# Kernel optimization log

Measured on AMD Instinct MI355X. Metric: run time of the kernel, lower is better.

Reference implementation:

```python
import jax, jax.numpy as jnp
import numpy as np

ALPHA = 0.2
N_ENT, N_TYP, N_REL, E = 100000, 1000, 200, 500000
D = 64          # nfeat1 = nfeat2 = nhid1 = nhid2 = relation_dim
NHEADS = 2      # forced by the tuple-unpack in the original forward


def _xavier(key, shape):
    fan_out, fan_in = shape[0], shape[-1]
    lim = 1.414 * np.sqrt(6.0 / (fan_in + fan_out))
    return jax.random.uniform(key, shape, jnp.float32, -lim, lim)


def setup_inputs() -> dict:
    key = jax.random.key(0)
    ks = jax.random.split(key, 32)
    inp = {
        "entity_embeddings": jax.random.normal(ks[0], (N_ENT, D), jnp.float32),
        "type_embed": jax.random.normal(ks[1], (N_TYP, D), jnp.float32),
        "relation_embed": jax.random.normal(ks[2], (N_REL, D), jnp.float32),
        "edge_list": jax.random.randint(ks[3], (2, E), 0, N_TYP),  # row0=src entity, row1=dst type; both in-range
        "edge_type": jax.random.randint(ks[4], (E,), 0, N_REL),
        "edge_embed": jax.random.normal(ks[5], (E, D), jnp.float32),
    }
    Din = 3 * D  # cat(x1[src], x2[dst], edge_embed)
    i = 6
    for h in range(NHEADS):
        inp[f"a_e{h}"] = _xavier(ks[i], (D, Din)); i += 1   # entity-side attention proj
        inp[f"v_e{h}"] = _xavier(ks[i], (1, D))[0]; i += 1  # entity-side score vector
        inp[f"a_t{h}"] = _xavier(ks[i], (D, Din)); i += 1   # type-side attention proj
        inp[f"v_t{h}"] = _xavier(ks[i], (1, D))[0]; i += 1
    Ho = NHEADS * D       # 128
    Dout = 3 * Ho         # out layer input cat dim
    inp["a_eo"] = _xavier(ks[i], (Ho, Dout)); i += 1
    inp["v_eo"] = _xavier(ks[i], (1, Ho))[0]; i += 1
    inp["a_to"] = _xavier(ks[i], (Ho, Dout)); i += 1
    inp["v_to"] = _xavier(ks[i], (1, Ho))[0]; i += 1
    inp["W"] = _xavier(ks[i], (D, Ho))  # relation_dim -> nheads*nhid1
    return inp


def _gat_e2t(x1, x2, src, dst, e, a_e, v_e, a_t, v_t, concat):
    """Bipartite sparse GAT layer (KBGAT-style, e2t variant).
    Message m = a @ cat(x1[src], x2[dst], edge_embed); score = exp(-leaky_relu(v . m));
    softmax-normalized scatter-aggregate to entity nodes (by src) and type nodes (by dst)."""
    d1, d2 = x1.shape[1], x2.shape[1]

    def agg(a, v, seg, nseg):
        a1, a2, a3 = a[:, :d1], a[:, d1:d1 + d2], a[:, d1 + d2:]
        # project nodes first, then gather (avoids materializing [E, 3d] cat)
        m = (x1 @ a1.T)[src] + (x2 @ a2.T)[dst] + e @ a3.T     # [E, h]
        s = jnp.exp(-jax.nn.leaky_relu(m @ v, ALPHA))          # [E] unnormalized attention
        num = jax.ops.segment_sum(m * s[:, None], seg, num_segments=nseg)
        den = jax.ops.segment_sum(s, seg, num_segments=nseg)
        h = num / jnp.where(den == 0, 1.0, den)[:, None]
        return jax.nn.elu(h) if concat else h

    h_e = agg(a_e, v_e, src, x1.shape[0])
    h_t = agg(a_t, v_t, dst, x2.shape[0])
    return h_e, h_t


def reference(entity_embeddings, type_embed, relation_embed, edge_list, edge_type, edge_embed,
              a_e0, v_e0, a_t0, v_t0, a_e1, v_e1, a_t1, v_t1,
              a_eo, v_eo, a_to, v_to, W):
    src, dst = edge_list[0], edge_list[1]
    # two attention heads (concat=True -> elu inside)
    h0e, h0t = _gat_e2t(entity_embeddings, type_embed, src, dst, edge_embed, a_e0, v_e0, a_t0, v_t0, True)
    h1e, h1t = _gat_e2t(entity_embeddings, type_embed, src, dst, edge_embed, a_e1, v_e1, a_t1, v_t1, True)
    x1 = jnp.concatenate([h0e, h1e], axis=1)  # [N_ENT, 2*nhid1]
    x2 = jnp.concatenate([h0t, h1t], axis=1)  # [N_TYP, 2*nhid2]
    # dropout is identity at inference
    out_rel = relation_embed @ W              # [N_REL, nheads*nhid1]
    e2 = out_rel[edge_type]                   # per-edge relation embedding
    o1, o2 = _gat_e2t(x1, x2, src, dst, e2, a_eo, v_eo, a_to, v_to, False)
    return jax.nn.elu(o1), jax.nn.elu(o2), out_rel
```

## Files before the change

### kernel.cpp

```cpp
#include <hip/hip_runtime.h>

#define ALPHA 0.2f
#define NT 1000
#define NRELC 200
#define NE 500000
#define N_ENT 100000
#define CH 4096
#define G 123

static constexpr size_t I_STARTS_SRC = 0;
static constexpr size_t I_STARTS_DST = 1001;
static constexpr size_t I_COLSUM     = 2002;
static constexpr size_t I_HIST2      = 4002;
static constexpr size_t I_BASE2      = 250002;
static constexpr size_t I_AB_SRC     = 496002;
static constexpr size_t I_AB_DST     = 1496002;

static constexpr size_t F_U1 = 2496004;
static constexpr size_t F_U2 = F_U1 + 768;
static constexpr size_t F_L1 = F_U2 + 768;
static constexpr size_t F_X1 = F_L1 + 4*130000;
static constexpr size_t F_X2 = F_X1 + 128000;
static constexpr size_t F_OR = F_X2 + 128000;
static constexpr size_t F_L2 = F_OR + 25600;
static constexpr size_t S2F = 283800;
static constexpr size_t WS_FLOATS = F_L2 + 2*S2F;

static constexpr size_t OUT_O2  = 12800000;
static constexpr size_t OUT_REL = 12928000;

__device__ __forceinline__ float eluf(float x) { return x > 0.f ? x : expm1f(x); }
__device__ __forceinline__ float scoref(float slin) {
  return expf(slin > 0.f ? -slin : -ALPHA * slin);
}

__global__ __launch_bounds__(256) void k_hist2(const int* __restrict__ src,
                                               const int* __restrict__ dst,
                                               int* __restrict__ ip) {
  __shared__ int h[NT];
  int bid = blockIdx.x;
  int side = bid >= G;
  int blk = bid - side * G;
  const int* keys = side ? dst : src;
  int j0 = blk * CH;
  int n = min(CH, NE - j0);
  for (int i = threadIdx.x; i < NT; i += 256) h[i] = 0;
  __syncthreads();
  for (int k = threadIdx.x; k < n; k += 256) atomicAdd(&h[keys[j0 + k]], 1);
  __syncthreads();
  int* row = ip + I_HIST2 + (size_t)(side * G + blk) * NT;
  for (int b = threadIdx.x; b < NT; b += 256) row[b] = h[b];
}

__global__ void k_colsum(int* __restrict__ ip) {
  int t = blockIdx.x * 256 + threadIdx.x;
  if (t >= 2 * NT) return;
  int side = t / NT, bin = t - side * NT;
  int s = 0;
  for (int blk = 0; blk < G; ++blk)
    s += ip[I_HIST2 + (size_t)(side * G + blk) * NT + bin];
  ip[I_COLSUM + t] = s;
}

__global__ void k_scan2b(int* __restrict__ ip) {
  __shared__ int buf[1024];
  int t = threadIdx.x;
  for (int side = 0; side < 2; ++side) {
    int v = (t < NT) ? ip[I_COLSUM + side * NT + t] : 0;
    buf[t] = v;
    __syncthreads();
    for (int off = 1; off < 1024; off <<= 1) {
      int x = (t >= off) ? buf[t - off] : 0;
      __syncthreads();
      buf[t] += x;
      __syncthreads();
    }
    int* st = ip + (side ? I_STARTS_DST : I_STARTS_SRC);
    if (t < NT) st[t] = buf[t] - v;
    if (t == NT - 1) st[NT] = buf[t];
    __syncthreads();
  }
}

__global__ void k_bases(int* __restrict__ ip) {
  int t = blockIdx.x * 256 + threadIdx.x;
  if (t >= 2 * NT) return;
  int side = t / NT, bin = t - side * NT;
  int run = ip[(side ? I_STARTS_DST : I_STARTS_SRC) + bin];
  for (int blk = 0; blk < G; ++blk) {
    size_t idx = I_HIST2 + (size_t)(side * G + blk) * NT + bin;
    int c = ip[idx];
    ip[idx + (I_BASE2 - I_HIST2)] = run;
    run += c;
  }
}

__global__ __launch_bounds__(256) void k_binscat(const int* __restrict__ src,
                                                 const int* __restrict__ dst,
                                                 const int* __restrict__ et,
                                                 int* __restrict__ ip) {
  __shared__ int2 bufs[CH];
  __shared__ int loff[1024];
  __shared__ int lcur[1024];
  __shared__ int gbase[1024];
  __shared__ int psum[256];
  int bid = blockIdx.x;
  int side = bid >= G;
  int blk = bid - side * G;
  const int* keys = side ? dst : src;
  const int* oths = side ? src : dst;
  int j0 = blk * CH;
  int n = min(CH, NE - j0);
  int t = threadIdx.x;

  for (int i = t; i < 1024; i += 256) lcur[i] = 0;
  __syncthreads();
  for (int k = t; k < n; k += 256) atomicAdd(&lcur[keys[j0 + k]], 1);
  __syncthreads();
  int c0 = lcur[4*t], c1 = lcur[4*t+1], c2 = lcur[4*t+2], c3 = lcur[4*t+3];
  int s = c0 + c1 + c2 + c3;
  psum[t] = s;
  __syncthreads();
  for (int off = 1; off < 256; off <<= 1) {
    int x = (t >= off) ? psum[t - off] : 0;
    __syncthreads();
    psum[t] += x;
    __syncthreads();
  }
  int base = psum[t] - s;
  loff[4*t]   = base;
  loff[4*t+1] = base + c0;
  loff[4*t+2] = base + c0 + c1;
  loff[4*t+3] = base + c0 + c1 + c2;
  lcur[4*t]   = loff[4*t];
  lcur[4*t+1] = loff[4*t+1];
  lcur[4*t+2] = loff[4*t+2];
  lcur[4*t+3] = loff[4*t+3];
  const int* brow = ip + I_BASE2 + (size_t)(side * G + blk) * NT;
  for (int b = t; b < NT; b += 256) gbase[b] = brow[b];
  __syncthreads();
  for (int k = t; k < n; k += 256) {
    int j = j0 + k;
    int b = keys[j];
    int pos = atomicAdd(&lcur[b], 1);
    bufs[pos] = make_int2(j | (b << 19), oths[j] | (et[j] << 16));
  }
  __syncthreads();
  int2* out = reinterpret_cast<int2*>(ip + (side ? I_AB_DST : I_AB_SRC));
  for (int k = t; k < n; k += 256) {
    int2 q = bufs[k];
    int b = q.x >> 19;
    int posg = gbase[b] + (k - loff[b]);
    out[posg] = make_int2(q.x & 0x7FFFF, q.y);
  }
}

__global__ void k_prep_u(const float* aE0, const float* vE0, const float* aT0, const float* vT0,
                         const float* aE1, const float* vE1, const float* aT1, const float* vT1,
                         const float* aEo, const float* vEo, const float* aTo, const float* vTo,
                         float* ws) {
  int t = blockIdx.x * blockDim.x + threadIdx.x;
  if (t < 768) {
    int c = t / 192, rem = t - c*192;
    int p = rem >> 6, k = rem & 63;
    const float* a = (c==0)?aE0:(c==1)?aT0:(c==2)?aE1:aT1;
    const float* v = (c==0)?vE0:(c==1)?vT0:(c==2)?vE1:vT1;
    float s = 0.f;
    for (int o = 0; o < 64; ++o) s += a[o*192 + p*64 + k] * v[o];
    ws[F_U1 + (size_t)(c*3+p)*64 + k] = s;
  } else if (t < 1536) {
    int tt = t - 768;
    int c = tt / 384, rem = tt - c*384;
    int p = rem >> 7, k = rem & 127;
    const float* a = c ? aTo : aEo;
    const float* v = c ? vTo : vEo;
    float s = 0.f;
    for (int o = 0; o < 128; ++o) s += a[o*384 + p*128 + k] * v[o];
    ws[F_U2 + (size_t)(c*3+p)*128 + k] = s;
  }
}

__global__ __launch_bounds__(256) void k_l1_proj(const float* Ent, const float* Typ,
                                                 const float* aE0, const float* aT0,
                                                 const float* aE1, const float* aT1,
                                                 float* ws) {
  int bid = blockIdx.x;
  int t = threadIdx.x;
  if (bid < 504) {
    __shared__ float xs[16][64];
    int c = bid / 126, rem = bid - c*126;
    int table = rem / 63, tile = rem - table*63;
    int i0 = tile * 16;
    const float* a = (c==0)?aE0:(c==1)?aT0:(c==2)?aE1:aT1;
    const float* x = table ? Typ : Ent;
    float* outb = ws + F_L1 + (size_t)c*130000 + (table ? 64000 : 0);
    for (int idx = t; idx < 1024; idx += 256) {
      int r = idx >> 6, k = idx & 63;
      int i = i0 + r;
      xs[r][k] = (i < NT) ? x[(size_t)i*64 + k] : 0.f;
    }
    __syncthreads();
    int o = t & 63, grp = t >> 6;
    const float* arow = a + o*192 + table*64;
    float acc0 = 0.f, acc1 = 0.f, acc2 = 0.f, acc3 = 0.f;
    #pragma unroll 8
    for (int k = 0; k < 64; ++k) {
      float av = arow[k];
      acc0 += xs[grp*4+0][k] * av;
      acc1 += xs[grp*4+1][k] * av;
      acc2 += xs[grp*4+2][k] * av;
      acc3 += xs[grp*4+3][k] * av;
    }
    int ib = i0 + grp*4;
    if (ib + 0 < NT) outb[(size_t)(ib+0)*64 + o] = acc0;
    if (ib + 1 < NT) outb[(size_t)(ib+1)*64 + o] = acc1;
    if (ib + 2 < NT) outb[(size_t)(ib+2)*64 + o] = acc2;
    if (ib + 3 < NT) outb[(size_t)(ib+3)*64 + o] = acc3;
  } else {
    int idx = (bid - 504) * 256 + t;
    if (idx >= 8000) return;
    int c = idx / 2000, rem = idx - c*2000;
    float* base = ws + F_L1 + (size_t)c * 130000;
    if (rem < 1000) {
      const float* x = Ent + (size_t)rem*64;
      const float* u = ws + F_U1 + (size_t)(c*3)*64;
      float s = 0.f;
      #pragma unroll
      for (int k = 0; k < 64; ++k) s += x[k]*u[k];
      base[128000 + rem] = s;
    } else {
      int i = rem - 1000;
      const float* x = Typ + (size_t)i*64;
      const float* u = ws + F_U1 + (size_t)(c*3+1)*64;
      float s = 0.f;
      #pragma unroll
      for (int k = 0; k < 64; ++k) s += x[k]*u[k];
      base[129000 + i] = s;
    }
  }
}

__global__ __launch_bounds__(256) void k_l1_acc(const float* __restrict__ Eemb,
                                                const float* aE0, const float* aT0,
                                                const float* aE1, const float* aT1,
                                                const int* __restrict__ ip,
                                                float* __restrict__ ws) {
  __shared__ float Tl[2][NT];
  __shared__ float cOthL[2][NT];
  __shared__ float accR[2][16][64];
  __shared__ float accE[2][64];
  __shared__ float red[256];
  __shared__ float denl[2];

  int side = blockIdx.x >= NT;
  int g = blockIdx.x - side * NT;
  int t = threadIdx.x;
  int sub = t & 15, slot = t >> 4;
  int c0 = side, c1 = side + 2;

  size_t othOff = side ? 128000 : 129000;
  size_t ownOff = side ? 129000 : 128000;
  for (int i = t; i < NT; i += 256) {
    Tl[0][i] = 0.f; Tl[1][i] = 0.f;
    cOthL[0][i] = ws[F_L1 + (size_t)c0*130000 + othOff + i];
    cOthL[1][i] = ws[F_L1 + (size_t)c1*130000 + othOff + i];
  }
  if (t < 2) denl[t] = 0.f;
  float ownA = ws[F_L1 + (size_t)c0*130000 + ownOff + g];
  float ownB = ws[F_L1 + (size_t)c1*130000 + ownOff + g];
  float4 w3A = reinterpret_cast<const float4*>(ws + F_U1 + (size_t)(c0*3+2)*64)[sub];
  float4 w3B = reinterpret_cast<const float4*>(ws + F_U1 + (size_t)(c1*3+2)*64)[sub];
  __syncthreads();

  int start = ip[(side ? I_STARTS_DST : I_STARTS_SRC) + g];
  int end   = ip[(side ? I_STARTS_DST : I_STARTS_SRC) + g + 1];
  const int2* ab = reinterpret_cast<const int2*>(ip + (side ? I_AB_DST : I_AB_SRC));
  const float4* EV = reinterpret_cast<const float4*>(Eemb);

  float4 acc0 = make_float4(0.f,0.f,0.f,0.f);
  float4 acc1 = make_float4(0.f,0.f,0.f,0.f);
  float d0 = 0.f, d1 = 0.f;

  int p = start + slot;
  for (; p + 48 < end; p += 64) {
    int2 q0 = ab[p], q1 = ab[p+16], q2 = ab[p+32], q3 = ab[p+48];
    float4 e0 = EV[(size_t)q0.x*16 + sub];
    float4 e1 = EV[(size_t)q1.x*16 + sub];
    float4 e2 = EV[(size_t)q2.x*16 + sub];
    float4 e3 = EV[(size_t)q3.x*16 + sub];
    float rA0 = e0.x*w3A.x + e0.y*w3A.y + e0.z*w3A.z + e0.w*w3A.w;
    float rB0 = e0.x*w3B.x + e0.y*w3B.y + e0.z*w3B.z + e0.w*w3B.w;
    float rA1 = e1.x*w3A.x + e1.y*w3A.y + e1.z*w3A.z + e1.w*w3A.w;
    float rB1 = e1.x*w3B.x + e1.y*w3B.y + e1.z*w3B.z + e1.w*w3B.w;
    float rA2 = e2.x*w3A.x + e2.y*w3A.y + e2.z*w3A.z + e2.w*w3A.w;
    float rB2 = e2.x*w3B.x + e2.y*w3B.y + e2.z*w3B.z + e2.w*w3B.w;
    float rA3 = e3.x*w3A.x + e3.y*w3A.y + e3.z*w3A.z + e3.w*w3A.w;
    float rB3 = e3.x*w3B.x + e3.y*w3B.y + e3.z*w3B.z + e3.w*w3B.w;
    #pragma unroll
    for (int sh = 1; sh < 16; sh <<= 1) {
      rA0 += __shfl_xor(rA0, sh, 16); rB0 += __shfl_xor(rB0, sh, 16);
      rA1 += __shfl_xor(rA1, sh, 16); rB1 += __shfl_xor(rB1, sh, 16);
      rA2 += __shfl_xor(rA2, sh, 16); rB2 += __shfl_xor(rB2, sh, 16);
      rA3 += __shfl_xor(rA3, sh, 16); rB3 += __shfl_xor(rB3, sh, 16);
    }
    int o0 = q0.y & 0xFFFF, o1 = q1.y & 0xFFFF, o2 = q2.y & 0xFFFF, o3 = q3.y & 0xFFFF;
    float sA0 = scoref(ownA + cOthL[0][o0] + rA0);
    float sB0 = scoref(ownB + cOthL[1][o0] + rB0);
    float sA1 = scoref(ownA + cOthL[0][o1] + rA1);
    float sB1 = scoref(ownB + cOthL[1][o1] + rB1);
    float sA2 = scoref(ownA + cOthL[0][o2] + rA2);
    float sB2 = scoref(ownB + cOthL[1][o2] + rB2);
    float sA3 = scoref(ownA + cOthL[0][o3] + rA3);
    float sB3 = scoref(ownB + cOthL[1][o3] + rB3);
    acc0.x += sA0*e0.x + sA1*e1.x + sA2*e2.x + sA3*e3.x;
    acc0.y += sA0*e0.y + sA1*e1.y + sA2*e2.y + sA3*e3.y;
    acc0.z += sA0*e0.z + sA1*e1.z + sA2*e2.z + sA3*e3.z;
    acc0.w += sA0*e0.w + sA1*e1.w + sA2*e2.w + sA3*e3.w;
    acc1.x += sB0*e0.x + sB1*e1.x + sB2*e2.x + sB3*e3.x;
    acc1.y += sB0*e0.y + sB1*e1.y + sB2*e2.y + sB3*e3.y;
    acc1.z += sB0*e0.z + sB1*e1.z + sB2*e2.z + sB3*e3.z;
    acc1.w += sB0*e0.w + sB1*e1.w + sB2*e2.w + sB3*e3.w;
    if (sub == 0) {
      atomicAdd(&Tl[0][o0], sA0); atomicAdd(&Tl[1][o0], sB0);
      atomicAdd(&Tl[0][o1], sA1); atomicAdd(&Tl[1][o1], sB1);
      atomicAdd(&Tl[0][o2], sA2); atomicAdd(&Tl[1][o2], sB2);
      atomicAdd(&Tl[0][o3], sA3); atomicAdd(&Tl[1][o3], sB3);
      d0 += sA0 + sA1 + sA2 + sA3;
      d1 += sB0 + sB1 + sB2 + sB3;
    }
  }
  for (; p < end; p += 16) {
    int2 q = ab[p];
    float4 ev = EV[(size_t)q.x*16 + sub];
    float rA = ev.x*w3A.x + ev.y*w3A.y + ev.z*w3A.z + ev.w*w3A.w;
    float rB = ev.x*w3B.x + ev.y*w3B.y + ev.z*w3B.z + ev.w*w3B.w;
    #pragma unroll
    for (int sh = 1; sh < 16; sh <<= 1) {
      rA += __shfl_xor(rA, sh, 16);
      rB += __shfl_xor(rB, sh, 16);
    }
    int oth = q.y & 0xFFFF;
    float sA = scoref(ownA + cOthL[0][oth] + rA);
    float sB = scoref(ownB + cOthL[1][oth] + rB);
    acc0.x += sA*ev.x; acc0.y += sA*ev.y; acc0.z += sA*ev.z; acc0.w += sA*ev.w;
    acc1.x += sB*ev.x; acc1.y += sB*ev.y; acc1.z += sB*ev.z; acc1.w += sB*ev.w;
    if (sub == 0) {
      atomicAdd(&Tl[0][oth], sA);
      atomicAdd(&Tl[1][oth], sB);
      d0 += sA; d1 += sB;
    }
  }
  *reinterpret_cast<float4*>(&accR[0][slot][sub*4]) = acc0;
  *reinterpret_cast<float4*>(&accR[1][slot][sub*4]) = acc1;
  if (sub == 0) { atomicAdd(&denl[0], d0); atomicAdd(&denl[1], d1); }
  __syncthreads();
  if (t < 128) {
    int ci = t >> 6, o = t & 63;
    float s = 0.f;
    #pragma unroll
    for (int sl = 0; sl < 16; ++sl) s += accR[ci][sl][o];
    accE[ci][o] = s;
  }
  __syncthreads();

  int o = t & 63, part = t >> 6;
  size_t othPOff = side ? 0 : 64000;
  size_t ownPOff = side ? 64000 : 0;
  #pragma unroll
  for (int ci = 0; ci < 2; ++ci) {
    int c = side + 2*ci;
    const float* Pc = ws + F_L1 + (size_t)c * 130000;
    const float* Poth = Pc + othPOff;
    float sum = 0.f;
    for (int dd = part*250; dd < part*250 + 250; ++dd)
      sum += Tl[ci][dd] * Poth[(size_t)dd*64 + o];
    red[t] = sum;
    __syncthreads();
    if (part == 0) {
      sum = red[o] + red[64+o] + red[128+o] + red[192+o];
      const float* a = (c==0)?aE0:(c==1)?aT0:(c==2)?aE1:aT1;
      const float* a3 = a + o*192 + 128;
      float acc = 0.f;
      #pragma unroll
      for (int k = 0; k < 64; ++k) acc += accE[ci][k]*a3[k];
      float den = denl[ci];
      float own = Pc[ownPOff + (size_t)g*64 + o];
      float num = sum + acc + den*own;
      float h = num / (den == 0.f ? 1.f : den);
      float* dst = ws + (side ? F_X2 : F_X1);
      dst[(size_t)g*128 + ci*64 + o] = eluf(h);
    }
    __syncthreads();
  }
}

__global__ void k_relW(const float* Rel, const float* W, float* ws, float* dout) {
  int t = blockIdx.x * blockDim.x + threadIdx.x;
  if (t >= NRELC*128) return;
  int r = t >> 7, o = t & 127;
  const float* x = Rel + (size_t)r*64;
  float s = 0.f;
  #pragma unroll
  for (int k = 0; k < 64; ++k) s += x[k] * W[(size_t)k*128 + o];
  ws[F_OR + t] = s;
  dout[OUT_REL + t] = s;
}

__global__ __launch_bounds__(256) void k_l2_proj(const float* aEo, const float* aTo,
                                                 float* ws) {
  int bid = blockIdx.x;
  int t = threadIdx.x;
  const float* x1 = ws + F_X1;
  const float* x2 = ws + F_X2;
  const float* orel = ws + F_OR;
  if (bid < 278) {
    __shared__ float xs[16][128];
    int c = bid / 139, rem = bid - c*139;
    const float* a = c ? aTo : aEo;
    float* cb = ws + F_L2 + (size_t)c * S2F;
    const float* x; int part, tile, nrows; float* outb;
    if (rem < 63)       { x = x1;   part = 0; tile = rem;       nrows = NT;    outb = cb; }
    else if (rem < 126) { x = x2;   part = 1; tile = rem - 63;  nrows = NT;    outb = cb + 128000; }
    else                { x = orel; part = 2; tile = rem - 126; nrows = NRELC; outb = cb + 256000; }
    int i0 = tile * 16;
    for (int idx = t; idx < 2048; idx += 256) {
      int r = idx >> 7, k = idx & 127;
      int i = i0 + r;
      xs[r][k] = (i < nrows) ? x[(size_t)i*128 + k] : 0.f;
    }
    __syncthreads();
    int o = t & 127, grp = t >> 7;
    const float* arow = a + (size_t)o*384 + part*128;
    float acc[8] = {0.f,0.f,0.f,0.f,0.f,0.f,0.f,0.f};
    #pragma unroll 4
    for (int k = 0; k < 128; ++k) {
      float av = arow[k];
      #pragma unroll
      for (int r = 0; r < 8; ++r)
        acc[r] += xs[grp*8+r][k] * av;
    }
    int ib = i0 + grp*8;
    #pragma unroll
    for (int r = 0; r < 8; ++r)
      if (ib + r < nrows) outb[(size_t)(ib+r)*128 + o] = acc[r];
  } else {
    int idx = (bid - 278) * 256 + t;
    if (idx >= 4400) return;
    int c = idx / 2200, rem = idx - c*2200;
    float* base = ws + F_L2 + (size_t)c * S2F;
    if (rem < 1000) {
      const float* u = ws + F_U2 + (size_t)(c*3)*128;
      const float* x = x1 + (size_t)rem*128;
      float s = 0.f;
      for (int k = 0; k < 128; ++k) s += x[k]*u[k];
      base[281600 + rem] = s;
    } else if (rem < 2000) {
      int i = rem - 1000;
      const float* u = ws + F_U2 + (size_t)(c*3+1)*128;
      const float* x = x2 + (size_t)i*128;
      float s = 0.f;
      for (int k = 0; k < 128; ++k) s += x[k]*u[k];
      base[282600 + i] = s;
    } else {
      int r = rem - 2000;
      const float* u = ws + F_U2 + (size_t)(c*3+2)*128;
      const float* x = orel + (size_t)r*128;
      float s = 0.f;
      for (int k = 0; k < 128; ++k) s += x[k]*u[k];
      base[283600 + r] = s;
    }
  }
}

__global__ __launch_bounds__(256) void k_l2_seg(const int* __restrict__ ip,
                                                float* __restrict__ ws,
                                                float* __restrict__ dout) {
  __shared__ float Tl[NT];
  __shared__ float Ul[NRELC];
  __shared__ float cOthL[NT];
  __shared__ float cRelL[NRELC];
  __shared__ float red[256];
  __shared__ float denl;

  int c = blockIdx.x >= NT;
  int g = blockIdx.x - c * NT;
  int t = threadIdx.x;
  float* base = ws + F_L2 + (size_t)c * S2F;

  size_t othOff = c ? 281600 : 282600;
  size_t ownOff = c ? 282600 : 281600;
  for (int i = t; i < NT; i += 256) { Tl[i] = 0.f; cOthL[i] = base[othOff + i]; }
  for (int i = t; i < NRELC; i += 256) { Ul[i] = 0.f; cRelL[i] = base[283600 + i]; }
  if (t == 0) denl = 0.f;
  float own = base[ownOff + g];
  __syncthreads();

  int start = ip[(c ? I_STARTS_DST : I_STARTS_SRC) + g];
  int end   = ip[(c ? I_STARTS_DST : I_STARTS_SRC) + g + 1];
  const int2* ab = reinterpret_cast<const int2*>(ip + (c ? I_AB_DST : I_AB_SRC));

  float dpart = 0.f;
  for (int p = start + t; p < end; p += 256) {
    int2 q = ab[p];
    int oth = q.y & 0xFFFF;
    int r = q.y >> 16;
    float sv = scoref(own + cOthL[oth] + cRelL[r]);
    atomicAdd(&Tl[oth], sv);
    atomicAdd(&Ul[r], sv);
    dpart += sv;
  }
  atomicAdd(&denl, dpart);
  __syncthreads();

  int o = t & 127, part = t >> 7;
  const float* Qoth = base + (c ? 0 : 128000);
  const float* R3 = base + 256000;
  float sum = 0.f;
  for (int dd = part*500; dd < part*500 + 500; ++dd)
    sum += Tl[dd] * Qoth[(size_t)dd*128 + o];
  for (int rr = part*100; rr < part*100 + 100; ++rr)
    sum += Ul[rr] * R3[(size_t)rr*128 + o];
  red[t] = sum;
  __syncthreads();
  if (part == 0) {
    sum = red[o] + red[128+o];
    float den = denl;
    float ownQ = base[(c ? 128000 : 0) + (size_t)g*128 + o];
    float num = sum + den*ownQ;
    float h = num / (den == 0.f ? 1.f : den);
    size_t off = c ? (OUT_O2 + (size_t)g*128 + o) : ((size_t)g*128 + o);
    dout[off] = eluf(h);
  }
}

extern "C" void kernel_launch(void* const* d_in, const int* in_sizes, int n_in,
                              void* d_out, int out_size, void* d_ws, size_t ws_size,
                              hipStream_t stream) {
  (void)in_sizes; (void)n_in;
  const float* Ent = (const float*)d_in[0];
  const float* Typ = (const float*)d_in[1];
  const float* Rel = (const float*)d_in[2];
  const int*   edge = (const int*)d_in[3];
  const int*   etyp = (const int*)d_in[4];
  const float* Eemb = (const float*)d_in[5];
  const float* aE0 = (const float*)d_in[6];
  const float* vE0 = (const float*)d_in[7];
  const float* aT0 = (const float*)d_in[8];
  const float* vT0 = (const float*)d_in[9];
  const float* aE1 = (const float*)d_in[10];
  const float* vE1 = (const float*)d_in[11];
  const float* aT1 = (const float*)d_in[12];
  const float* vT1 = (const float*)d_in[13];
  const float* aEo = (const float*)d_in[14];
  const float* vEo = (const float*)d_in[15];
  const float* aTo = (const float*)d_in[16];
  const float* vTo = (const float*)d_in[17];
  const float* W   = (const float*)d_in[18];
  float* ws  = (float*)d_ws;
  int*   ip  = (int*)d_ws;
  float* out = (float*)d_out;
  const int* srcA = edge;
  const int* dstA = edge + NE;

  if (ws_size < WS_FLOATS * sizeof(float)) return;

  hipMemsetAsync(d_out, 0, (size_t)out_size * sizeof(float), stream);

  k_hist2  <<<2*G, 256, 0, stream>>>(srcA, dstA, ip);
  k_colsum <<<8, 256, 0, stream>>>(ip);
  k_scan2b <<<1, 1024, 0, stream>>>(ip);
  k_bases  <<<8, 256, 0, stream>>>(ip);
  k_binscat<<<2*G, 256, 0, stream>>>(srcA, dstA, etyp, ip);
  k_prep_u <<<6, 256, 0, stream>>>(aE0,vE0,aT0,vT0,aE1,vE1,aT1,vT1,aEo,vEo,aTo,vTo,ws);
  k_l1_proj<<<536, 256, 0, stream>>>(Ent, Typ, aE0, aT0, aE1, aT1, ws);
  k_l1_acc <<<2000, 256, 0, stream>>>(Eemb, aE0, aT0, aE1, aT1, ip, ws);
  k_relW   <<<100, 256, 0, stream>>>(Rel, W, ws, out);
  k_l2_proj<<<296, 256, 0, stream>>>(aEo, aTo, ws);
  k_l2_seg <<<2000, 256, 0, stream>>>(ip, ws, out);
}
```

Before: 262.5 us.

## Pair segments per block in layer-2 aggregation, alias shared memory, halve binning chunk

The layer-2 segment kernel now handles two adjacent nodes per block, so each projection row read from Qoth and R3 serves both nodes and the block count is halved. The layer-1 accumulation kernel reuses one flat shared buffer, with the reduction scratch overlapping the score tables after an extra barrier, which cuts LDS use and may allow more resident blocks. The binning chunk size is halved and the grid doubled, with workspace offsets moved to fit the larger histogram. The costs are an extra per-edge branch in layer 2, less parallelism when segments are small, and one more sync in layer 1.

```diff
diff --git a/kernel.cpp b/kernel.cpp
--- a/kernel.cpp
+++ b/kernel.cpp
@@ -5,18 +5,18 @@
 #define NRELC 200
 #define NE 500000
 #define N_ENT 100000
-#define CH 4096
-#define G 123
+#define CH 2048
+#define G 245
 
 static constexpr size_t I_STARTS_SRC = 0;
 static constexpr size_t I_STARTS_DST = 1001;
 static constexpr size_t I_COLSUM     = 2002;
 static constexpr size_t I_HIST2      = 4002;
-static constexpr size_t I_BASE2      = 250002;
-static constexpr size_t I_AB_SRC     = 496002;
-static constexpr size_t I_AB_DST     = 1496002;
-
-static constexpr size_t F_U1 = 2496004;
+static constexpr size_t I_BASE2      = 494002;
+static constexpr size_t I_AB_SRC     = 984002;
+static constexpr size_t I_AB_DST     = 1984002;
+
+static constexpr size_t F_U1 = 2984004;
 static constexpr size_t F_U2 = F_U1 + 768;
 static constexpr size_t F_L1 = F_U2 + 768;
 static constexpr size_t F_X1 = F_L1 + 4*130000;
@@ -245,12 +245,14 @@
                                                 const float* aE1, const float* aT1,
                                                 const int* __restrict__ ip,
                                                 float* __restrict__ ws) {
-  __shared__ float Tl[2][NT];
-  __shared__ float cOthL[2][NT];
-  __shared__ float accR[2][16][64];
-  __shared__ float accE[2][64];
-  __shared__ float red[256];
-  __shared__ float denl[2];
+  __shared__ float smem[4434];
+  float* TlB   = smem;
+  float* cOth0 = smem + 2000;
+  float* cOth1 = smem + 3000;
+  float* accRf = smem + 2000;
+  float* accEf = smem + 4048;
+  float* redf  = smem + 4176;
+  float* denf  = smem + 4432;
 
   int side = blockIdx.x >= NT;
   int g = blockIdx.x - side * NT;
@@ -261,11 +263,11 @@
   size_t othOff = side ? 128000 : 129000;
   size_t ownOff = side ? 129000 : 128000;
   for (int i = t; i < NT; i += 256) {
-    Tl[0][i] = 0.f; Tl[1][i] = 0.f;
-    cOthL[0][i] = ws[F_L1 + (size_t)c0*130000 + othOff + i];
-    cOthL[1][i] = ws[F_L1 + (size_t)c1*130000 + othOff + i];
-  }
-  if (t < 2) denl[t] = 0.f;
+    TlB[i] = 0.f; TlB[1000 + i] = 0.f;
+    cOth0[i] = ws[F_L1 + (size_t)c0*130000 + othOff + i];
+    cOth1[i] = ws[F_L1 + (size_t)c1*130000 + othOff + i];
+  }
+  if (t < 2) denf[t] = 0.f;
   float ownA = ws[F_L1 + (size_t)c0*130000 + ownOff + g];
   float ownB = ws[F_L1 + (size_t)c1*130000 + ownOff + g];
   float4 w3A = reinterpret_cast<const float4*>(ws + F_U1 + (size_t)(c0*3+2)*64)[sub];
@@ -304,14 +306,14 @@
       rA3 += __shfl_xor(rA3, sh, 16); rB3 += __shfl_xor(rB3, sh, 16);
     }
     int o0 = q0.y & 0xFFFF, o1 = q1.y & 0xFFFF, o2 = q2.y & 0xFFFF, o3 = q3.y & 0xFFFF;
-    float sA0 = scoref(ownA + cOthL[0][o0] + rA0);
-    float sB0 = scoref(ownB + cOthL[1][o0] + rB0);
-    float sA1 = scoref(ownA + cOthL[0][o1] + rA1);
-    float sB1 = scoref(ownB + cOthL[1][o1] + rB1);
-    float sA2 = scoref(ownA + cOthL[0][o2] + rA2);
-    float sB2 = scoref(ownB + cOthL[1][o2] + rB2);
-    float sA3 = scoref(ownA + cOthL[0][o3] + rA3);
-    float sB3 = scoref(ownB + cOthL[1][o3] + rB3);
+    float sA0 = scoref(ownA + cOth0[o0] + rA0);
+    float sB0 = scoref(ownB + cOth1[o0] + rB0);
+    float sA1 = scoref(ownA + cOth0[o1] + rA1);
+    float sB1 = scoref(ownB + cOth1[o1] + rB1);
+    float sA2 = scoref(ownA + cOth0[o2] + rA2);
+    float sB2 = scoref(ownB + cOth1[o2] + rB2);
+    float sA3 = scoref(ownA + cOth0[o3] + rA3);
+    float sB3 = scoref(ownB + cOth1[o3] + rB3);
     acc0.x += sA0*e0.x + sA1*e1.x + sA2*e2.x + sA3*e3.x;
     acc0.y += sA0*e0.y + sA1*e1.y + sA2*e2.y + sA3*e3.y;
     acc0.z += sA0*e0.z + sA1*e1.z + sA2*e2.z + sA3*e3.z;
@@ -321,10 +323,10 @@
     acc1.z += sB0*e0.z + sB1*e1.z + sB2*e2.z + sB3*e3.z;
     acc1.w += sB0*e0.w + sB1*e1.w + sB2*e2.w + sB3*e3.w;
     if (sub == 0) {
-      atomicAdd(&Tl[0][o0], sA0); atomicAdd(&Tl[1][o0], sB0);
-      atomicAdd(&Tl[0][o1], sA1); atomicAdd(&Tl[1][o1], sB1);
-      atomicAdd(&Tl[0][o2], sA2); atomicAdd(&Tl[1][o2], sB2);
-      atomicAdd(&Tl[0][o3], sA3); atomicAdd(&Tl[1][o3], sB3);
+      atomicAdd(&TlB[o0], sA0); atomicAdd(&TlB[1000+o0], sB0);
+      atomicAdd(&TlB[o1], sA1); atomicAdd(&TlB[1000+o1], sB1);
+      atomicAdd(&TlB[o2], sA2); atomicAdd(&TlB[1000+o2], sB2);
+      atomicAdd(&TlB[o3], sA3); atomicAdd(&TlB[1000+o3], sB3);
       d0 += sA0 + sA1 + sA2 + sA3;
       d1 += sB0 + sB1 + sB2 + sB3;
     }
@@ -340,26 +342,27 @@
       rB += __shfl_xor(rB, sh, 16);
     }
     int oth = q.y & 0xFFFF;
-    float sA = scoref(ownA + cOthL[0][oth] + rA);
-    float sB = scoref(ownB + cOthL[1][oth] + rB);
+    float sA = scoref(ownA + cOth0[oth] + rA);
+    float sB = scoref(ownB + cOth1[oth] + rB);
     acc0.x += sA*ev.x; acc0.y += sA*ev.y; acc0.z += sA*ev.z; acc0.w += sA*ev.w;
     acc1.x += sB*ev.x; acc1.y += sB*ev.y; acc1.z += sB*ev.z; acc1.w += sB*ev.w;
     if (sub == 0) {
-      atomicAdd(&Tl[0][oth], sA);
-      atomicAdd(&Tl[1][oth], sB);
+      atomicAdd(&TlB[oth], sA);
+      atomicAdd(&TlB[1000+oth], sB);
       d0 += sA; d1 += sB;
     }
   }
-  *reinterpret_cast<float4*>(&accR[0][slot][sub*4]) = acc0;
-  *reinterpret_cast<float4*>(&accR[1][slot][sub*4]) = acc1;
-  if (sub == 0) { atomicAdd(&denl[0], d0); atomicAdd(&denl[1], d1); }
+  __syncthreads();
+  *reinterpret_cast<float4*>(&accRf[slot*64 + sub*4])        = acc0;
+  *reinterpret_cast<float4*>(&accRf[1024 + slot*64 + sub*4]) = acc1;
+  if (sub == 0) { atomicAdd(&denf[0], d0); atomicAdd(&denf[1], d1); }
   __syncthreads();
   if (t < 128) {
     int ci = t >> 6, o = t & 63;
     float s = 0.f;
     #pragma unroll
-    for (int sl = 0; sl < 16; ++sl) s += accR[ci][sl][o];
-    accE[ci][o] = s;
+    for (int sl = 0; sl < 16; ++sl) s += accRf[ci*1024 + sl*64 + o];
+    accEf[ci*64 + o] = s;
   }
   __syncthreads();
 
@@ -373,17 +376,17 @@
     const float* Poth = Pc + othPOff;
     float sum = 0.f;
     for (int dd = part*250; dd < part*250 + 250; ++dd)
-      sum += Tl[ci][dd] * Poth[(size_t)dd*64 + o];
-    red[t] = sum;
+      sum += TlB[ci*1000 + dd] * Poth[(size_t)dd*64 + o];
+    redf[t] = sum;
     __syncthreads();
     if (part == 0) {
-      sum = red[o] + red[64+o] + red[128+o] + red[192+o];
+      sum = redf[o] + redf[64+o] + redf[128+o] + redf[192+o];
       const float* a = (c==0)?aE0:(c==1)?aT0:(c==2)?aE1:aT1;
       const float* a3 = a + o*192 + 128;
       float acc = 0.f;
       #pragma unroll
-      for (int k = 0; k < 64; ++k) acc += accE[ci][k]*a3[k];
-      float den = denl[ci];
+      for (int k = 0; k < 64; ++k) acc += accEf[ci*64 + k]*a3[k];
+      float den = denf[ci];
       float own = Pc[ownPOff + (size_t)g*64 + o];
       float num = sum + acc + den*own;
       float h = num / (den == 0.f ? 1.f : den);
@@ -475,62 +478,73 @@
 __global__ __launch_bounds__(256) void k_l2_seg(const int* __restrict__ ip,
                                                 float* __restrict__ ws,
                                                 float* __restrict__ dout) {
-  __shared__ float Tl[NT];
-  __shared__ float Ul[NRELC];
+  __shared__ float Tl[2][NT];
+  __shared__ float Ul[2][NRELC];
   __shared__ float cOthL[NT];
   __shared__ float cRelL[NRELC];
-  __shared__ float red[256];
-  __shared__ float denl;
-
-  int c = blockIdx.x >= NT;
-  int g = blockIdx.x - c * NT;
+  __shared__ float red[2][256];
+  __shared__ float denl[2];
+
+  int c = blockIdx.x >= 500;
+  int gp = blockIdx.x - c * 500;
+  int g0 = gp * 2;
   int t = threadIdx.x;
   float* base = ws + F_L2 + (size_t)c * S2F;
 
   size_t othOff = c ? 281600 : 282600;
   size_t ownOff = c ? 282600 : 281600;
-  for (int i = t; i < NT; i += 256) { Tl[i] = 0.f; cOthL[i] = base[othOff + i]; }
-  for (int i = t; i < NRELC; i += 256) { Ul[i] = 0.f; cRelL[i] = base[283600 + i]; }
-  if (t == 0) denl = 0.f;
-  float own = base[ownOff + g];
-  __syncthreads();
-
-  int start = ip[(c ? I_STARTS_DST : I_STARTS_SRC) + g];
-  int end   = ip[(c ? I_STARTS_DST : I_STARTS_SRC) + g + 1];
+  for (int i = t; i < NT; i += 256) { Tl[0][i] = 0.f; Tl[1][i] = 0.f; cOthL[i] = base[othOff + i]; }
+  for (int i = t; i < NRELC; i += 256) { Ul[0][i] = 0.f; Ul[1][i] = 0.f; cRelL[i] = base[283600 + i]; }
+  if (t < 2) denl[t] = 0.f;
+  float own0 = base[ownOff + g0];
+  float own1 = base[ownOff + g0 + 1];
+  __syncthreads();
+
+  const int* st = ip + (c ? I_STARTS_DST : I_STARTS_SRC);
+  int s0 = st[g0], split = st[g0 + 1], e1 = st[g0 + 2];
   const int2* ab = reinterpret_cast<const int2*>(ip + (c ? I_AB_DST : I_AB_SRC));
 
-  float dpart = 0.f;
-  for (int p = start + t; p < end; p += 256) {
+  float d0 = 0.f, d1 = 0.f;
+  for (int p = s0 + t; p < e1; p += 256) {
     int2 q = ab[p];
     int oth = q.y & 0xFFFF;
     int r = q.y >> 16;
-    float sv = scoref(own + cOthL[oth] + cRelL[r]);
-    atomicAdd(&Tl[oth], sv);
-    atomicAdd(&Ul[r], sv);
-    dpart += sv;
-  }
-  atomicAdd(&denl, dpart);
+    int ls = p >= split;
+    float sv = scoref((ls ? own1 : own0) + cOthL[oth] + cRelL[r]);
+    atomicAdd(&Tl[ls][oth], sv);
+    atomicAdd(&Ul[ls][r], sv);
+    if (ls) d1 += sv; else d0 += sv;
+  }
+  atomicAdd(&denl[0], d0);
+  atomicAdd(&denl[1], d1);
   __syncthreads();
 
   int o = t & 127, part = t >> 7;
   const float* Qoth = base + (c ? 0 : 128000);
   const float* R3 = base + 256000;
-  float sum = 0.f;
-  for (int dd = part*500; dd < part*500 + 500; ++dd)
-    sum += Tl[dd] * Qoth[(size_t)dd*128 + o];
-  for (int rr = part*100; rr < part*100 + 100; ++rr)
-    sum += Ul[rr] * R3[(size_t)rr*128 + o];
-  red[t] = sum;
-  __syncthreads();
-  if (part == 0) {
-    sum = red[o] + red[128+o];
-    float den = denl;
-    float ownQ = base[(c ? 128000 : 0) + (size_t)g*128 + o];
-    float num = sum + den*ownQ;
-    float h = num / (den == 0.f ? 1.f : den);
-    size_t off = c ? (OUT_O2 + (size_t)g*128 + o) : ((size_t)g*128 + o);
-    dout[off] = eluf(h);
-  }
+  float sum0 = 0.f, sum1 = 0.f;
+  for (int dd = part*500; dd < part*500 + 500; ++dd) {
+    float qv = Qoth[(size_t)dd*128 + o];
+    sum0 += Tl[0][dd] * qv;
+    sum1 += Tl[1][dd] * qv;
+  }
+  for (int rr = part*100; rr < part*100 + 100; ++rr) {
+    float qv = R3[(size_t)rr*128 + o];
+    sum0 += Ul[0][rr] * qv;
+    sum1 += Ul[1][rr] * qv;
+  }
+  red[0][t] = sum0;
+  red[1][t] = sum1;
+  __syncthreads();
+  int li = part;
+  float den = denl[li];
+  float sum = red[li][o] + red[li][128 + o];
+  int gw = g0 + li;
+  float ownQ = base[(c ? 128000 : 0) + (size_t)gw*128 + o];
+  float num = sum + den * ownQ;
+  float h = num / (den == 0.f ? 1.f : den);
+  size_t off = c ? (OUT_O2 + (size_t)gw*128 + o) : ((size_t)gw*128 + o);
+  dout[off] = eluf(h);
 }
 
 extern "C" void kernel_launch(void* const* d_in, const int* in_sizes, int n_in,
@@ -576,5 +590,5 @@
   k_l1_acc <<<2000, 256, 0, stream>>>(Eemb, aE0, aT0, aE1, aT1, ip, ws);
   k_relW   <<<100, 256, 0, stream>>>(Rel, W, ws, out);
   k_l2_proj<<<296, 256, 0, stream>>>(aEo, aTo, ws);
-  k_l2_seg <<<2000, 256, 0, stream>>>(ip, ws, out);
-}
+  k_l2_seg <<<1000, 256, 0, stream>>>(ip, ws, out);
+}
```

After: 253.1 us, median of 3. 1.04x faster.
